# Optimization experiments

Measured on AMD Instinct MI355X. Metric: run time of the kernel, lower is better.

## Reference

```python
import jax, jax.numpy as jnp
import numpy as np

HEAD_SIZE = 64

def setup_inputs() -> dict:
    key = jax.random.key(0)
    k1, k2, k3, k4 = jax.random.split(key, 4)
    B, T, D = 4, 4096, 768
    x = jax.random.normal(k1, (B, T, D), dtype=jnp.float32)
    Wq = jax.random.normal(k2, (D, HEAD_SIZE), dtype=jnp.float32) * (1.0 / np.sqrt(D))
    Wk = jax.random.normal(k3, (D, HEAD_SIZE), dtype=jnp.float32) * (1.0 / np.sqrt(D))
    Wv = jax.random.normal(k4, (D, HEAD_SIZE), dtype=jnp.float32) * (1.0 / np.sqrt(D))
    return {"x": x, "Wq": Wq, "Wk": Wk, "Wv": Wv}

def reference(x, Wq, Wk, Wv):
    # q,k,v: [B, T, H]
    q = jnp.einsum('btd,dh->bth', x, Wq)
    k = jnp.einsum('btd,dh->bth', x, Wk)
    v = jnp.einsum('btd,dh->bth', x, Wv)
    # scores: [B, T, T]; causal mask via lower-triangular band, -inf elsewhere
    scores = jnp.einsum('bqh,bkh->bqk', q, k)
    T = x.shape[1]
    causal = jnp.tril(jnp.ones((T, T), dtype=bool))  # band_part(ones, -1, 0)
    scores = jnp.where(causal[None, :, :], scores, -jnp.inf)
    attn = jax.nn.softmax(scores / np.sqrt(HEAD_SIZE), axis=-1)
    # dropout is identity in eval mode
    return jnp.einsum('bqk,bkh->bqh', attn, v)
```

## Files before the change

kernel.cpp:

```cpp
#include <hip/hip_runtime.h>
#include <math.h>

typedef __attribute__((ext_vector_type(8))) short short8;
typedef __attribute__((ext_vector_type(4))) float f32x4;
typedef unsigned short ushort_t;

#define TSEQ   4096
#define NBATCH 4
#define DMODEL 768
#define HS     64
#define KSPLIT 4

static __device__ __forceinline__ ushort_t f2bf(float f) {
  union { float f; unsigned u; } v; v.f = f;
  unsigned r = v.u + 0x7fffu + ((v.u >> 16) & 1u);
  return (ushort_t)(r >> 16);
}
static __device__ __forceinline__ float bf2f(ushort_t u) {
  union { unsigned u; float f; } v; v.u = ((unsigned)u) << 16; return v.f;
}

#define MFMA16(a,b,c) __builtin_amdgcn_mfma_f32_16x16x32_bf16((a),(b),(c),0,0,0)

__global__ __launch_bounds__(256) void wprep(
    const float* __restrict__ Wq, const float* __restrict__ Wk,
    const float* __restrict__ Wv, ushort_t* __restrict__ Wt)
{
  __shared__ float lds[64 * 65];
  const int m = blockIdx.x / 12, kc = blockIdx.x % 12, k0 = kc * 64;
  const float* W = (m == 0) ? Wq : (m == 1) ? Wk : Wv;
  const int tid = threadIdx.x;
#pragma unroll
  for (int i = 0; i < 16; i++) {
    const int row = i * 4 + (tid >> 6), col = tid & 63;
    lds[row * 65 + col] = W[(size_t)(k0 + row) * HS + col];
  }
  __syncthreads();
#pragma unroll
  for (int i = 0; i < 16; i++) {
    const int n = i * 4 + (tid >> 6), kk = tid & 63;
    Wt[(size_t)(m * 64 + n) * DMODEL + k0 + kk] = f2bf(lds[kk * 65 + n]);
  }
}

__global__ __launch_bounds__(256, 2) void qkv_mfma(
    const float* __restrict__ x, const ushort_t* __restrict__ Wt,
    ushort_t* __restrict__ q, ushort_t* __restrict__ kO, ushort_t* __restrict__ vT)
{
  __shared__ __align__(16) ushort_t sA[2][32 * 72];
  __shared__ __align__(16) ushort_t sB[2][192 * 64];

  const int tid  = threadIdx.x;
  const int w    = tid >> 6;
  const int lane = tid & 63;
  const int l16  = lane & 15, quad = lane >> 4;
  const int M0   = blockIdx.x * 32;

  const int arow = tid >> 3, acol = (tid & 7) * 8;
  const float* ax = x + (size_t)(M0 + arow) * DMODEL + acol;

  const int bcol_l = lane >> 3;
  const int bkoff  = (((lane & 7) ^ (bcol_l & 7)) << 3);

  f32x4 acc[2][3];
#pragma unroll
  for (int mt = 0; mt < 2; mt++)
#pragma unroll
    for (int nt = 0; nt < 3; nt++) acc[mt][nt] = (f32x4){0.f, 0.f, 0.f, 0.f};

  {
#pragma unroll
    for (int j = 0; j < 6; j++) {
      const int colb = w * 48 + j * 8;
      __builtin_amdgcn_global_load_lds(
          (const __attribute__((address_space(1))) ushort_t*)
              (Wt + (size_t)(colb + bcol_l) * DMODEL + bkoff),
          (__attribute__((address_space(3))) ushort_t*)(&sB[0][colb * 64]),
          16, 0, 0);
    }
    const float4 f0 = *(const float4*)(ax);
    const float4 f1 = *(const float4*)(ax + 4);
    short8 p;
    p[0]=f2bf(f0.x); p[1]=f2bf(f0.y); p[2]=f2bf(f0.z); p[3]=f2bf(f0.w);
    p[4]=f2bf(f1.x); p[5]=f2bf(f1.y); p[6]=f2bf(f1.z); p[7]=f2bf(f1.w);
    *(short8*)(&sA[0][arow * 72 + acol]) = p;
  }

  for (int ks = 0; ks < DMODEL / 64; ks++) {
    const int cur = ks & 1, nxt = cur ^ 1;
    __syncthreads();

    float4 f0n, f1n;
    if (ks < DMODEL / 64 - 1) {
#pragma unroll
      for (int j = 0; j < 6; j++) {
        const int colb = w * 48 + j * 8;
        __builtin_amdgcn_global_load_lds(
            (const __attribute__((address_space(1))) ushort_t*)
                (Wt + (size_t)(colb + bcol_l) * DMODEL + (ks + 1) * 64 + bkoff),
            (__attribute__((address_space(3))) ushort_t*)(&sB[nxt][colb * 64]),
            16, 0, 0);
      }
      f0n = *(const float4*)(ax + (ks + 1) * 64);
      f1n = *(const float4*)(ax + (ks + 1) * 64 + 4);
    }

    const ushort_t* sAc = &sA[cur][0];
    const ushort_t* sBc = &sB[cur][0];
#pragma unroll
    for (int kc = 0; kc < 2; kc++) {
      const short8 a0 = *(const short8*)(sAc + (l16)      * 72 + kc * 32 + quad * 8);
      const short8 a1 = *(const short8*)(sAc + (16 + l16) * 72 + kc * 32 + quad * 8);
      const int kswz = (kc * 32 + quad * 8) ^ ((l16 & 7) << 3);
#pragma unroll
      for (int nt = 0; nt < 3; nt++) {
        const short8 bf =
            *(const short8*)(sBc + (w * 48 + nt * 16 + l16) * 64 + kswz);
        acc[0][nt] = MFMA16(a0, bf, acc[0][nt]);
        acc[1][nt] = MFMA16(a1, bf, acc[1][nt]);
      }
    }

    if (ks < DMODEL / 64 - 1) {
      short8 p;
      p[0]=f2bf(f0n.x); p[1]=f2bf(f0n.y); p[2]=f2bf(f0n.z); p[3]=f2bf(f0n.w);
      p[4]=f2bf(f1n.x); p[5]=f2bf(f1n.y); p[6]=f2bf(f1n.z); p[7]=f2bf(f1n.w);
      *(short8*)(&sA[nxt][arow * 72 + acol]) = p;
    }
  }

#pragma unroll
  for (int mt = 0; mt < 2; mt++)
#pragma unroll
    for (int nt = 0; nt < 3; nt++) {
      const int gnt = w * 3 + nt;
      const int mat = gnt >> 2;
      const int col = (gnt & 3) * 16 + l16;
      if (mat == 0) {
#pragma unroll
        for (int r = 0; r < 4; r++)
          q[(size_t)(M0 + mt * 16 + quad * 4 + r) * HS + col] =
              f2bf(acc[mt][nt][r] * 0.125f);
      } else if (mat == 1) {
#pragma unroll
        for (int r = 0; r < 4; r++)
          kO[(size_t)(M0 + mt * 16 + quad * 4 + r) * HS + col] =
              f2bf(acc[mt][nt][r]);
      }
    }
  __syncthreads();
  float* vls = (float*)&sA[0][0];
#pragma unroll
  for (int mt = 0; mt < 2; mt++)
#pragma unroll
    for (int nt = 0; nt < 3; nt++) {
      const int gnt = w * 3 + nt;
      if ((gnt >> 2) == 2) {
        const int vcol = (gnt & 3) * 16 + l16;
#pragma unroll
        for (int r = 0; r < 4; r++)
          vls[(mt * 16 + quad * 4 + r) * 65 + vcol] = acc[mt][nt][r];
      }
    }
  __syncthreads();
  const int d = tid >> 2, seg = tid & 3;
  short8 pk;
#pragma unroll
  for (int i = 0; i < 8; i++) pk[i] = (short)f2bf(vls[(seg * 8 + i) * 65 + d]);
  *(short8*)(vT + ((size_t)(M0 >> 12) * HS + d) * TSEQ + (M0 & (TSEQ - 1)) + seg * 8) = pk;
}

#define KP 72
__global__ __launch_bounds__(128) void attn_part(
    const ushort_t* __restrict__ q, const ushort_t* __restrict__ k,
    const ushort_t* __restrict__ vT, float* __restrict__ ML, ushort_t* __restrict__ OP)
{
  __shared__ __align__(16) ushort_t sK[64 * KP];
  __shared__ __align__(16) ushort_t sV[64 * KP];
  __shared__ __align__(16) ushort_t sP[2][16 * KP];

  const int idx  = blockIdx.x;
  const int s    = idx & 3;
  const int b    = (idx >> 2) & 3;
  const int jt   = 127 - (idx >> 4);
  const int tid  = threadIdx.x;
  const int w    = tid >> 6;
  const int lane = tid & 63;
  const int l16  = lane & 15, quad = lane >> 4;
  const int R0   = jt * 32 + w * 16;

  const ushort_t* qg = q  + (size_t)b * TSEQ * HS;
  const ushort_t* kg = k  + (size_t)b * TSEQ * HS;
  const ushort_t* vg = vT + (size_t)b * HS * TSEQ;

  const short8 qf0 = *(const short8*)(qg + (R0 + l16) * HS +      quad * 8);
  const short8 qf1 = *(const short8*)(qg + (R0 + l16) * HS + 32 + quad * 8);

  f32x4 o[4];
#pragma unroll
  for (int dt = 0; dt < 4; dt++) o[dt] = (f32x4){0.f, 0.f, 0.f, 0.f};
  float mrow = -INFINITY, lrow = 0.f;

  const int nkt = jt / 2 + 1;
  short8 kpre[4], vpre[4];
  int kt = s;
  if (kt < nkt) {
    const int k0 = kt * 64;
#pragma unroll
    for (int i = 0; i < 4; i++) {
      const int c = i * 128 + tid, key = c >> 3, ch = c & 7;
      kpre[i] = *(const short8*)(kg + (size_t)(k0 + key) * HS + ch * 8);
      vpre[i] = *(const short8*)(vg + (size_t)key * TSEQ + k0 + ch * 8);
    }
  }
  for (; kt < nkt; kt += KSPLIT) {
    const int k0 = kt * 64;
    __syncthreads();
#pragma unroll
    for (int i = 0; i < 4; i++) {
      const int c = i * 128 + tid, key = c >> 3, ch = c & 7;
      *(short8*)(sK + key * KP + ch * 8) = kpre[i];
      *(short8*)(sV + key * KP + ch * 8) = vpre[i];
    }
    if (kt + KSPLIT < nkt) {
      const int kn = (kt + KSPLIT) * 64;
#pragma unroll
      for (int i = 0; i < 4; i++) {
        const int c = i * 128 + tid, key = c >> 3, ch = c & 7;
        kpre[i] = *(const short8*)(kg + (size_t)(kn + key) * HS + ch * 8);
        vpre[i] = *(const short8*)(vg + (size_t)key * TSEQ + kn + ch * 8);
      }
    }
    __syncthreads();
    f32x4 sT[4];
#pragma unroll
    for (int ct = 0; ct < 4; ct++) {
      sT[ct] = (f32x4){0.f, 0.f, 0.f, 0.f};
      const short8 kfa = *(const short8*)(sK + (ct * 16 + l16) * KP +      quad * 8);
      const short8 kfb = *(const short8*)(sK + (ct * 16 + l16) * KP + 32 + quad * 8);
      sT[ct] = MFMA16(kfa, qf0, sT[ct]);
      sT[ct] = MFMA16(kfb, qf1, sT[ct]);
    }
    if (k0 + 63 > R0) {
      const int qrow = R0 + l16;
#pragma unroll
      for (int ct = 0; ct < 4; ct++)
#pragma unroll
        for (int r = 0; r < 4; r++)
          sT[ct][r] = (k0 + ct * 16 + quad * 4 + r <= qrow) ? sT[ct][r] : -INFINITY;
    }
    float tm = -INFINITY;
#pragma unroll
    for (int ct = 0; ct < 4; ct++)
#pragma unroll
      for (int r = 0; r < 4; r++) tm = fmaxf(tm, sT[ct][r]);
    tm = fmaxf(tm, __shfl_xor(tm, 16));
    tm = fmaxf(tm, __shfl_xor(tm, 32));
    const float mn = fmaxf(mrow, tm);
    const float al = __expf(mrow - mn);
    mrow = mn;
    float ps = 0.f;
#pragma unroll
    for (int ct = 0; ct < 4; ct++)
#pragma unroll
      for (int r = 0; r < 4; r++) { sT[ct][r] = __expf(sT[ct][r] - mn); ps += sT[ct][r]; }
    ps += __shfl_xor(ps, 16);
    ps += __shfl_xor(ps, 32);
    lrow = lrow * al + ps;
    ushort_t* Pw = &sP[w][0];
#pragma unroll
    for (int ct = 0; ct < 4; ct++) {
      ushort4 pk;
      pk.x = f2bf(sT[ct][0]); pk.y = f2bf(sT[ct][1]);
      pk.z = f2bf(sT[ct][2]); pk.w = f2bf(sT[ct][3]);
      *(ushort4*)(Pw + l16 * KP + ct * 16 + quad * 4) = pk;
    }
    float alo[4];
#pragma unroll
    for (int r = 0; r < 4; r++) alo[r] = __shfl(al, quad * 4 + r);
#pragma unroll
    for (int dt = 0; dt < 4; dt++)
#pragma unroll
      for (int r = 0; r < 4; r++) o[dt][r] *= alo[r];
    const short8 pf0 = *(const short8*)(Pw + l16 * KP +      quad * 8);
    const short8 pf1 = *(const short8*)(Pw + l16 * KP + 32 + quad * 8);
#pragma unroll
    for (int dt = 0; dt < 4; dt++) {
      const short8 vfa = *(const short8*)(sV + (dt * 16 + l16) * KP +      quad * 8);
      const short8 vfb = *(const short8*)(sV + (dt * 16 + l16) * KP + 32 + quad * 8);
      o[dt] = MFMA16(pf0, vfa, o[dt]);
      o[dt] = MFMA16(pf1, vfb, o[dt]);
    }
  }

  const size_t base = ((size_t)(b * KSPLIT + s) * TSEQ);
  if (quad == 0) {
    ML[(base + R0 + l16) * 2 + 0] = mrow;
    ML[(base + R0 + l16) * 2 + 1] = lrow;
  }
#pragma unroll
  for (int dt = 0; dt < 4; dt++)
#pragma unroll
    for (int r = 0; r < 4; r++)
      OP[(base + R0 + quad * 4 + r) * HS + dt * 16 + l16] = f2bf(o[dt][r]);
}

__global__ __launch_bounds__(256) void attn_merge(
    const float* __restrict__ ML, const ushort_t* __restrict__ OP,
    float* __restrict__ out)
{
  const int row = blockIdx.x * 16 + (threadIdx.x >> 4);
  const int b   = row >> 12, t = row & (TSEQ - 1);
  const int d0  = (threadIdx.x & 15) * 4;
  float m[KSPLIT], l[KSPLIT];
  float M = -INFINITY;
#pragma unroll
  for (int ss = 0; ss < KSPLIT; ss++) {
    const size_t i = ((size_t)(b * KSPLIT + ss) * TSEQ + t);
    m[ss] = ML[i * 2]; l[ss] = ML[i * 2 + 1];
    M = fmaxf(M, m[ss]);
  }
  float den = 0.f;
  float4 num = make_float4(0.f, 0.f, 0.f, 0.f);
#pragma unroll
  for (int ss = 0; ss < KSPLIT; ss++) {
    const float a = __expf(m[ss] - M);
    den += l[ss] * a;
    const size_t i = ((size_t)(b * KSPLIT + ss) * TSEQ + t);
    const ushort4 u = *(const ushort4*)(OP + i * HS + d0);
    num.x += a * bf2f(u.x); num.y += a * bf2f(u.y);
    num.z += a * bf2f(u.z); num.w += a * bf2f(u.w);
  }
  const float inv = 1.f / den;
  *(float4*)(out + (size_t)row * HS + d0) =
      make_float4(num.x * inv, num.y * inv, num.z * inv, num.w * inv);
}

extern "C" void kernel_launch(void* const* d_in, const int* in_sizes, int n_in,
                              void* d_out, int out_size, void* d_ws, size_t ws_size,
                              hipStream_t stream) {
  const float* x  = (const float*)d_in[0];
  const float* Wq = (const float*)d_in[1];
  const float* Wk = (const float*)d_in[2];
  const float* Wv = (const float*)d_in[3];
  float* out = (float*)d_out;

  char* ws = (char*)d_ws;
  ushort_t* Wt = (ushort_t*)ws;
  ushort_t* qb = (ushort_t*)(ws + 294912);
  ushort_t* kb = (ushort_t*)(ws + 294912 + 2097152);
  ushort_t* vb = (ushort_t*)(ws + 294912 + 2 * 2097152);
  float*    ml = (float*)   (ws + 294912 + 3 * 2097152);
  ushort_t* op = (ushort_t*)(ws + 294912 + 3 * 2097152 + 524288);

  wprep<<<36, 256, 0, stream>>>(Wq, Wk, Wv, Wt);
  qkv_mfma<<<(NBATCH * TSEQ) / 32, 256, 0, stream>>>(x, Wt, qb, kb, vb);
  attn_part<<<128 * NBATCH * KSPLIT, 128, 0, stream>>>(qb, kb, vb, ml, op);
  attn_merge<<<1024, 256, 0, stream>>>(ml, op, out);
}
```

Baseline: 131.1 us.

## Use direct global-to-LDS loads with XOR-swizzled K/V layout and 64-row query tiles

The QKV projection now writes K and V^T in an XOR-swizzled column order, which lets the attention kernel fetch K/V tiles with global_load_lds straight into unpadded, double-buffered LDS instead of staging them through registers. The attention block grows to 4 waves covering 64 query rows, so each K/V tile is reused by twice as many rows, and one of the two barriers per iteration is removed. The aim is to cut register pressure, staging stores and redundant K/V traffic. The costs are fewer blocks, which lowers parallelism in the causal split, and correctness now depends on the asynchronous LDS loads being complete by the time the barrier is passed.

Result: faster. 128.0 us (-2.3%).

```diff
diff --git a/kernel.cpp b/kernel.cpp
--- a/kernel.cpp
+++ b/kernel.cpp
@@ -135,17 +135,20 @@
     for (int nt = 0; nt < 3; nt++) {
       const int gnt = w * 3 + nt;
       const int mat = gnt >> 2;
-      const int col = (gnt & 3) * 16 + l16;
       if (mat == 0) {
+        const int col = (gnt & 3) * 16 + l16;
 #pragma unroll
         for (int r = 0; r < 4; r++)
           q[(size_t)(M0 + mt * 16 + quad * 4 + r) * HS + col] =
               f2bf(acc[mt][nt][r] * 0.125f);
       } else if (mat == 1) {
-#pragma unroll
-        for (int r = 0; r < 4; r++)
-          kO[(size_t)(M0 + mt * 16 + quad * 4 + r) * HS + col] =
-              f2bf(acc[mt][nt][r]);
+        const int cb2 = (gnt & 3) * 2 + (l16 >> 3);
+#pragma unroll
+        for (int r = 0; r < 4; r++) {
+          const int trow  = M0 + mt * 16 + quad * 4 + r;
+          const int cphys = ((cb2 ^ (trow & 7)) << 3) | (l16 & 7);
+          kO[(size_t)trow * HS + cphys] = f2bf(acc[mt][nt][r]);
+        }
       }
     }
   __syncthreads();
@@ -167,77 +170,98 @@
   short8 pk;
 #pragma unroll
   for (int i = 0; i < 8; i++) pk[i] = (short)f2bf(vls[(seg * 8 + i) * 65 + d]);
-  *(short8*)(vT + ((size_t)(M0 >> 12) * HS + d) * TSEQ + (M0 & (TSEQ - 1)) + seg * 8) = pk;
+  {
+    const int t0  = M0 & (TSEQ - 1);
+    const int tb  = t0 & ~63;
+    const int kb  = ((t0 & 63) >> 3) + seg;
+    const int kbp = kb ^ (d & 7);
+    *(short8*)(vT + ((size_t)(M0 >> 12) * HS + d) * TSEQ + tb + kbp * 8) = pk;
+  }
 }
 
 #define KP 72
-__global__ __launch_bounds__(128) void attn_part(
+__global__ __launch_bounds__(256, 3) void attn_part(
     const ushort_t* __restrict__ q, const ushort_t* __restrict__ k,
     const ushort_t* __restrict__ vT, float* __restrict__ ML, ushort_t* __restrict__ OP)
 {
-  __shared__ __align__(16) ushort_t sK[64 * KP];
-  __shared__ __align__(16) ushort_t sV[64 * KP];
-  __shared__ __align__(16) ushort_t sP[2][16 * KP];
+  __shared__ __align__(16) ushort_t sK[2][64 * 64];
+  __shared__ __align__(16) ushort_t sV[2][64 * 64];
+  __shared__ __align__(16) ushort_t sP[4][16 * KP];
 
   const int idx  = blockIdx.x;
   const int s    = idx & 3;
   const int b    = (idx >> 2) & 3;
-  const int jt   = 127 - (idx >> 4);
+  const int jt   = 63 - (idx >> 4);
   const int tid  = threadIdx.x;
   const int w    = tid >> 6;
   const int lane = tid & 63;
   const int l16  = lane & 15, quad = lane >> 4;
-  const int R0   = jt * 32 + w * 16;
+  const int R0   = jt * 64 + w * 16;
 
   const ushort_t* qg = q  + (size_t)b * TSEQ * HS;
   const ushort_t* kg = k  + (size_t)b * TSEQ * HS;
   const ushort_t* vg = vT + (size_t)b * HS * TSEQ;
 
-  const short8 qf0 = *(const short8*)(qg + (R0 + l16) * HS +      quad * 8);
-  const short8 qf1 = *(const short8*)(qg + (R0 + l16) * HS + 32 + quad * 8);
+  const short8 qf0 = *(const short8*)(qg + (size_t)(R0 + l16) * HS +      quad * 8);
+  const short8 qf1 = *(const short8*)(qg + (size_t)(R0 + l16) * HS + 32 + quad * 8);
 
   f32x4 o[4];
 #pragma unroll
   for (int dt = 0; dt < 4; dt++) o[dt] = (f32x4){0.f, 0.f, 0.f, 0.f};
   float mrow = -INFINITY, lrow = 0.f;
 
-  const int nkt = jt / 2 + 1;
-  short8 kpre[4], vpre[4];
-  int kt = s;
+  const int nkt = jt + 1;
+  const int srow = lane >> 3;
+  const int scol = (lane & 7) * 8;
+
+  int kt = s, cur = 0;
   if (kt < nkt) {
     const int k0 = kt * 64;
 #pragma unroll
-    for (int i = 0; i < 4; i++) {
-      const int c = i * 128 + tid, key = c >> 3, ch = c & 7;
-      kpre[i] = *(const short8*)(kg + (size_t)(k0 + key) * HS + ch * 8);
-      vpre[i] = *(const short8*)(vg + (size_t)key * TSEQ + k0 + ch * 8);
+    for (int j = 0; j < 2; j++) {
+      const int r0 = w * 16 + j * 8;
+      __builtin_amdgcn_global_load_lds(
+          (const __attribute__((address_space(1))) ushort_t*)
+              (kg + (size_t)(k0 + r0 + srow) * HS + scol),
+          (__attribute__((address_space(3))) ushort_t*)(&sK[0][r0 * 64]),
+          16, 0, 0);
+      __builtin_amdgcn_global_load_lds(
+          (const __attribute__((address_space(1))) ushort_t*)
+              (vg + (size_t)(r0 + srow) * TSEQ + k0 + scol),
+          (__attribute__((address_space(3))) ushort_t*)(&sV[0][r0 * 64]),
+          16, 0, 0);
     }
   }
   for (; kt < nkt; kt += KSPLIT) {
     const int k0 = kt * 64;
     __syncthreads();
-#pragma unroll
-    for (int i = 0; i < 4; i++) {
-      const int c = i * 128 + tid, key = c >> 3, ch = c & 7;
-      *(short8*)(sK + key * KP + ch * 8) = kpre[i];
-      *(short8*)(sV + key * KP + ch * 8) = vpre[i];
-    }
     if (kt + KSPLIT < nkt) {
       const int kn = (kt + KSPLIT) * 64;
 #pragma unroll
-      for (int i = 0; i < 4; i++) {
-        const int c = i * 128 + tid, key = c >> 3, ch = c & 7;
-        kpre[i] = *(const short8*)(kg + (size_t)(kn + key) * HS + ch * 8);
-        vpre[i] = *(const short8*)(vg + (size_t)key * TSEQ + kn + ch * 8);
-      }
-    }
-    __syncthreads();
+      for (int j = 0; j < 2; j++) {
+        const int r0 = w * 16 + j * 8;
+        __builtin_amdgcn_global_load_lds(
+            (const __attribute__((address_space(1))) ushort_t*)
+                (kg + (size_t)(kn + r0 + srow) * HS + scol),
+            (__attribute__((address_space(3))) ushort_t*)(&sK[cur ^ 1][r0 * 64]),
+            16, 0, 0);
+        __builtin_amdgcn_global_load_lds(
+            (const __attribute__((address_space(1))) ushort_t*)
+                (vg + (size_t)(r0 + srow) * TSEQ + kn + scol),
+            (__attribute__((address_space(3))) ushort_t*)(&sV[cur ^ 1][r0 * 64]),
+            16, 0, 0);
+      }
+    }
+    const ushort_t* sKc = &sK[cur][0];
+    const ushort_t* sVc = &sV[cur][0];
+    const int sw = (l16 & 7) << 3;
+
     f32x4 sT[4];
 #pragma unroll
     for (int ct = 0; ct < 4; ct++) {
       sT[ct] = (f32x4){0.f, 0.f, 0.f, 0.f};
-      const short8 kfa = *(const short8*)(sK + (ct * 16 + l16) * KP +      quad * 8);
-      const short8 kfb = *(const short8*)(sK + (ct * 16 + l16) * KP + 32 + quad * 8);
+      const short8 kfa = *(const short8*)(sKc + (ct * 16 + l16) * 64 + ((quad * 8)      ^ sw));
+      const short8 kfb = *(const short8*)(sKc + (ct * 16 + l16) * 64 + ((32 + quad * 8) ^ sw));
       sT[ct] = MFMA16(kfa, qf0, sT[ct]);
       sT[ct] = MFMA16(kfb, qf1, sT[ct]);
     }
@@ -286,11 +310,12 @@
     const short8 pf1 = *(const short8*)(Pw + l16 * KP + 32 + quad * 8);
 #pragma unroll
     for (int dt = 0; dt < 4; dt++) {
-      const short8 vfa = *(const short8*)(sV + (dt * 16 + l16) * KP +      quad * 8);
-      const short8 vfb = *(const short8*)(sV + (dt * 16 + l16) * KP + 32 + quad * 8);
+      const short8 vfa = *(const short8*)(sVc + (dt * 16 + l16) * 64 + ((quad * 8)      ^ sw));
+      const short8 vfb = *(const short8*)(sVc + (dt * 16 + l16) * 64 + ((32 + quad * 8) ^ sw));
       o[dt] = MFMA16(pf0, vfa, o[dt]);
       o[dt] = MFMA16(pf1, vfb, o[dt]);
     }
+    cur ^= 1;
   }
 
   const size_t base = ((size_t)(b * KSPLIT + s) * TSEQ);
@@ -355,6 +380,6 @@
 
   wprep<<<36, 256, 0, stream>>>(Wq, Wk, Wv, Wt);
   qkv_mfma<<<(NBATCH * TSEQ) / 32, 256, 0, stream>>>(x, Wt, qb, kb, vb);
-  attn_part<<<128 * NBATCH * KSPLIT, 128, 0, stream>>>(qb, kb, vb, ml, op);
+  attn_part<<<64 * NBATCH * KSPLIT, 256, 0, stream>>>(qb, kb, vb, ml, op);
   attn_merge<<<1024, 256, 0, stream>>>(ml, op, out);
 }
```
